# Kernel optimization log

Hardware: AMD Instinct MI355X
Metric: run time of the kernel (lower is better)

The kernel has to match this reference:

```python
import jax, jax.numpy as jnp
import numpy as np

N_NODES = 50000
N_EDGES = 800000
IN_CH = 128
HID_CH = 128   # factor(2) * out_channels(64)
OUT_CH = 64


def setup_inputs() -> dict:
    key = jax.random.key(0)
    k_x, k_e, k_w1, k_w2 = jax.random.split(key, 4)
    x = jax.random.normal(k_x, (N_NODES, IN_CH), dtype=jnp.float32)
    edge_index = jax.random.randint(k_e, (2, N_EDGES), 0, N_NODES, dtype=jnp.int32)
    # GCNConv weights (Glorot) and biases, layer1: in->2*out, layer2: 2*out->out
    s1 = float(np.sqrt(6.0 / (IN_CH + HID_CH)))
    s2 = float(np.sqrt(6.0 / (HID_CH + OUT_CH)))
    W1 = jax.random.uniform(k_w1, (IN_CH, HID_CH), jnp.float32, -s1, s1)
    b1 = jnp.zeros((HID_CH,), jnp.float32)
    W2 = jax.random.uniform(k_w2, (HID_CH, OUT_CH), jnp.float32, -s2, s2)
    b2 = jnp.zeros((OUT_CH,), jnp.float32)
    return {"x": x, "edge_index": edge_index, "W1": W1, "b1": b1, "W2": W2, "b2": b2}


def reference(x, edge_index, W1, b1, W2, b2):
    N = x.shape[0]
    src, dst = edge_index[0], edge_index[1]
    # add self loops (PyG GCNConv default)
    loop = jnp.arange(N, dtype=edge_index.dtype)
    src2 = jnp.concatenate([src, loop])
    dst2 = jnp.concatenate([dst, loop])
    # symmetric normalization D^-1/2 (A+I) D^-1/2
    deg = jax.ops.segment_sum(jnp.ones_like(src2, dtype=x.dtype), dst2, num_segments=N)
    deg_inv_sqrt = jnp.where(deg > 0, jax.lax.rsqrt(jnp.maximum(deg, 1e-12)), 0.0)
    norm = deg_inv_sqrt[src2] * deg_inv_sqrt[dst2]  # [E+N]

    def gcn_conv(h, W, b):
        h = h @ W                                   # [N, C_out]
        msg = h[src2] * norm[:, None]               # gather + scale
        agg = jax.ops.segment_sum(msg, dst2, num_segments=N)  # scatter-add
        return agg + b

    h = jax.nn.relu(gcn_conv(x, W1, b1))
    h = jax.nn.relu(gcn_conv(h, W2, b2))
    return h
```

## Files before the change

kernel.cpp:

```cpp
#include <hip/hip_runtime.h>
#include <math.h>

#define NN 50000
#define NE 800000
#define NB 391
#define CAP 4096
#define CHUNK 4096

typedef __attribute__((ext_vector_type(8))) short s8v;
typedef __attribute__((ext_vector_type(8))) unsigned short u16x8;
typedef __attribute__((ext_vector_type(4))) float f4v;

__device__ inline short bf16_rtn(float f) {
  unsigned u = __builtin_bit_cast(unsigned, f);
  u = (u + 0x7FFFu + ((u >> 16) & 1u)) >> 16;
  return (short)u;
}
__device__ inline float bf16_to_f(unsigned short h) {
  unsigned u = ((unsigned)h) << 16;
  return __builtin_bit_cast(float, u);
}

__global__ __launch_bounds__(512) void k_bucketA(const int* __restrict__ src,
                                                 const int* __restrict__ dst,
                                                 int* __restrict__ bcnt,
                                                 unsigned* __restrict__ ebuf, int E) {
  __shared__ int h[NB], lofs[NB], gbase[NB], lcur[NB];
  __shared__ unsigned staged[CHUNK];
  const int tid = threadIdx.x;
  const int e0 = blockIdx.x * CHUNK;
  const int nE = min(CHUNK, E - e0);
  for (int i = tid; i < NB; i += 512) { h[i] = 0; lcur[i] = 0; }
  __syncthreads();
  for (int i = tid; i < nE; i += 512) atomicAdd(&h[dst[e0 + i] >> 7], 1);
  __syncthreads();
  if (tid < 64) {
    int carry = 0;
    for (int c = 0; c < 7; ++c) {
      int idx = c * 64 + tid;
      int v = (idx < NB) ? h[idx] : 0;
      int s = v;
#pragma unroll
      for (int o = 1; o < 64; o <<= 1) {
        int t = __shfl_up(s, o);
        if (tid >= o) s += t;
      }
      if (idx < NB) lofs[idx] = carry + s - v;
      carry += __shfl(s, 63);
    }
  }
  __syncthreads();
  for (int i = tid; i < NB; i += 512)
    gbase[i] = h[i] ? (i * CAP + atomicAdd(&bcnt[i], h[i])) : 0;
  __syncthreads();
  for (int i = tid; i < nE; i += 512) {
    int d = dst[e0 + i];
    int s = src[e0 + i];
    int b = d >> 7;
    int pos = lofs[b] + atomicAdd(&lcur[b], 1);
    staged[pos] = ((unsigned)b << 23) | ((unsigned)(d & 127) << 16) | (unsigned)s;
  }
  __syncthreads();
  for (int i = tid; i < nE; i += 512) {
    unsigned v = staged[i];
    int b = v >> 23;
    ebuf[gbase[b] + (i - lofs[b])] = v;
  }
}

__global__ __launch_bounds__(256) void k_bucketB(const unsigned* __restrict__ ebuf,
                                                 const int* __restrict__ bcnt,
                                                 unsigned short* __restrict__ col,
                                                 int* __restrict__ rps,
                                                 int* __restrict__ rpe,
                                                 float* __restrict__ dinv) {
  __shared__ int h[128], ofs[128], lc[128];
  const int tid = threadIdx.x;
  const int b = blockIdx.x;
  const int base = b * CAP;
  const int cntE = bcnt[b];
  const int node0 = b << 7;
  const int nloc = min(128, NN - node0);
  if (tid < 128) { h[tid] = 0; lc[tid] = 0; }
  __syncthreads();
  for (int i = tid; i < cntE; i += 256) atomicAdd(&h[(ebuf[base + i] >> 16) & 127], 1);
  __syncthreads();
  if (tid < 64) {
    int carry = 0;
    for (int c = 0; c < 2; ++c) {
      int idx = c * 64 + tid;
      int v = h[idx];
      int s = v;
#pragma unroll
      for (int o = 1; o < 64; o <<= 1) {
        int t = __shfl_up(s, o);
        if (tid >= o) s += t;
      }
      ofs[idx] = carry + s - v;
      carry += __shfl(s, 63);
    }
  }
  __syncthreads();
  if (tid < nloc) {
    rps[node0 + tid] = base + ofs[tid];
    rpe[node0 + tid] = base + ofs[tid] + h[tid];
    dinv[node0 + tid] = rsqrtf((float)h[tid] + 1.0f);
  }
  __syncthreads();
  for (int i = tid; i < cntE; i += 256) {
    unsigned v = ebuf[base + i];
    int l = (v >> 16) & 127;
    int p = atomicAdd(&lc[l], 1);
    col[base + ofs[l] + p] = (unsigned short)(v & 0xFFFFu);
  }
}

template <int N>
__global__ __launch_bounds__(512) void k_gemm_mfma(const float* __restrict__ X,
                                                   const float* __restrict__ W,
                                                   const float* __restrict__ dinv,
                                                   unsigned short* __restrict__ H,
                                                   int M) {
  constexpr int NT = N / 16;
  constexpr int NSLOT = 4 * NT * 64;
  __shared__ short s_hi[NSLOT * 8];
  __shared__ short s_lo[NSLOT * 8];
  const int tid = threadIdx.x;

  for (int slot = tid; slot < NSLOT; slot += 512) {
    int lane = slot & 63;
    int frag = slot >> 6;
    int nt = frag % NT;
    int kt = frag / NT;
    int colb = nt * 16 + (lane & 15);
    int kb = kt * 32 + (lane >> 4) * 8;
    s8v hi, lo;
#pragma unroll
    for (int j = 0; j < 8; ++j) {
      float w = W[(size_t)(kb + j) * N + colb];
      short h = bf16_rtn(w);
      hi[j] = h;
      lo[j] = bf16_rtn(w - bf16_to_f((unsigned short)h));
    }
    *(s8v*)&s_hi[slot * 8] = hi;
    *(s8v*)&s_lo[slot * 8] = lo;
  }
  __syncthreads();

  const int wave = tid >> 6, lane = tid & 63;
  const int row0 = blockIdx.x * 128 + wave * 16;
  int arow = row0 + (lane & 15);
  if (arow >= M) arow = M - 1;
  const float* xr = X + (size_t)arow * 128 + (lane >> 4) * 8;

  f4v acc[NT];
#pragma unroll
  for (int nt = 0; nt < NT; ++nt) acc[nt] = (f4v){0.f, 0.f, 0.f, 0.f};

#pragma unroll
  for (int kt = 0; kt < 4; ++kt) {
    float4 a0 = *(const float4*)(xr + kt * 32);
    float4 a1 = *(const float4*)(xr + kt * 32 + 4);
    float af[8] = {a0.x, a0.y, a0.z, a0.w, a1.x, a1.y, a1.z, a1.w};
    s8v ah, al;
#pragma unroll
    for (int j = 0; j < 8; ++j) {
      short h = bf16_rtn(af[j]);
      ah[j] = h;
      al[j] = bf16_rtn(af[j] - bf16_to_f((unsigned short)h));
    }
#pragma unroll
    for (int nt = 0; nt < NT; ++nt) {
      int base = ((kt * NT + nt) * 64 + lane) * 8;
      s8v bh = *(const s8v*)&s_hi[base];
      s8v bl = *(const s8v*)&s_lo[base];
      acc[nt] = __builtin_amdgcn_mfma_f32_16x16x32_bf16(ah, bh, acc[nt], 0, 0, 0);
      acc[nt] = __builtin_amdgcn_mfma_f32_16x16x32_bf16(ah, bl, acc[nt], 0, 0, 0);
      acc[nt] = __builtin_amdgcn_mfma_f32_16x16x32_bf16(al, bh, acc[nt], 0, 0, 0);
    }
  }

  const int orow = row0 + (lane >> 4) * 4;
  const int ocol = lane & 15;
  float sc[4];
#pragma unroll
  for (int r = 0; r < 4; ++r) sc[r] = (orow + r < M) ? dinv[orow + r] : 0.f;
#pragma unroll
  for (int nt = 0; nt < NT; ++nt)
#pragma unroll
    for (int r = 0; r < 4; ++r)
      if (orow + r < M)
        H[(size_t)(orow + r) * N + nt * 16 + ocol] =
            (unsigned short)bf16_rtn(acc[nt][r] * sc[r]);
}

template <int N>
__global__ __launch_bounds__(512) void k_gemm_mfma_bf16A(
    const unsigned short* __restrict__ A, const float* __restrict__ W,
    const float* __restrict__ dinv, unsigned short* __restrict__ H, int M) {
  constexpr int NT = N / 16;
  constexpr int NSLOT = 4 * NT * 64;
  __shared__ short s_hi[NSLOT * 8];
  __shared__ short s_lo[NSLOT * 8];
  const int tid = threadIdx.x;

  for (int slot = tid; slot < NSLOT; slot += 512) {
    int lane = slot & 63;
    int frag = slot >> 6;
    int nt = frag % NT;
    int kt = frag / NT;
    int colb = nt * 16 + (lane & 15);
    int kb = kt * 32 + (lane >> 4) * 8;
    s8v hi, lo;
#pragma unroll
    for (int j = 0; j < 8; ++j) {
      float w = W[(size_t)(kb + j) * N + colb];
      short h = bf16_rtn(w);
      hi[j] = h;
      lo[j] = bf16_rtn(w - bf16_to_f((unsigned short)h));
    }
    *(s8v*)&s_hi[slot * 8] = hi;
    *(s8v*)&s_lo[slot * 8] = lo;
  }
  __syncthreads();

  const int wave = tid >> 6, lane = tid & 63;
  const int row0 = blockIdx.x * 128 + wave * 16;
  int arow = row0 + (lane & 15);
  if (arow >= M) arow = M - 1;
  const unsigned short* xr = A + (size_t)arow * 128 + (lane >> 4) * 8;

  f4v acc[NT];
#pragma unroll
  for (int nt = 0; nt < NT; ++nt) acc[nt] = (f4v){0.f, 0.f, 0.f, 0.f};

#pragma unroll
  for (int kt = 0; kt < 4; ++kt) {
    s8v ah = __builtin_bit_cast(s8v, *(const u16x8*)(xr + kt * 32));
#pragma unroll
    for (int nt = 0; nt < NT; ++nt) {
      int base = ((kt * NT + nt) * 64 + lane) * 8;
      s8v bh = *(const s8v*)&s_hi[base];
      s8v bl = *(const s8v*)&s_lo[base];
      acc[nt] = __builtin_amdgcn_mfma_f32_16x16x32_bf16(ah, bh, acc[nt], 0, 0, 0);
      acc[nt] = __builtin_amdgcn_mfma_f32_16x16x32_bf16(ah, bl, acc[nt], 0, 0, 0);
    }
  }

  const int orow = row0 + (lane >> 4) * 4;
  const int ocol = lane & 15;
  float sc[4];
#pragma unroll
  for (int r = 0; r < 4; ++r) sc[r] = (orow + r < M) ? dinv[orow + r] : 0.f;
#pragma unroll
  for (int nt = 0; nt < NT; ++nt)
#pragma unroll
    for (int r = 0; r < 4; ++r)
      if (orow + r < M)
        H[(size_t)(orow + r) * N + nt * 16 + ocol] =
            (unsigned short)bf16_rtn(acc[nt][r] * sc[r]);
}

template <int COUT, bool STORE_BF16>
__global__ __launch_bounds__(256) void k_agg(const unsigned short* __restrict__ H,
                                             const unsigned short* __restrict__ col,
                                             const int* __restrict__ rps,
                                             const int* __restrict__ rpe,
                                             const float* __restrict__ dinv,
                                             const float* __restrict__ bias,
                                             void* __restrict__ outv, int n) {
  const int TPN = COUT / 8;
  const int NPB = 256 / TPN;
  int node = blockIdx.x * NPB + threadIdx.x / TPN;
  int cg = (threadIdx.x % TPN) * 8;
  if (node >= n) return;
  float di = dinv[node];
  float acc[8];
  u16x8 hv = *(const u16x8*)(H + (size_t)node * COUT + cg);
#pragma unroll
  for (int q = 0; q < 8; ++q) acc[q] = bf16_to_f(hv[q]);
  int j = rps[node];
  int end = rpe[node];
  for (; j + 4 <= end; j += 4) {
    int s0 = col[j + 0], s1 = col[j + 1], s2 = col[j + 2], s3 = col[j + 3];
    u16x8 a = *(const u16x8*)(H + (size_t)s0 * COUT + cg);
    u16x8 b = *(const u16x8*)(H + (size_t)s1 * COUT + cg);
    u16x8 c = *(const u16x8*)(H + (size_t)s2 * COUT + cg);
    u16x8 d = *(const u16x8*)(H + (size_t)s3 * COUT + cg);
#pragma unroll
    for (int q = 0; q < 8; ++q)
      acc[q] += bf16_to_f(a[q]) + bf16_to_f(b[q]) + bf16_to_f(c[q]) + bf16_to_f(d[q]);
  }
  for (; j < end; ++j) {
    u16x8 a = *(const u16x8*)(H + (size_t)col[j] * COUT + cg);
#pragma unroll
    for (int q = 0; q < 8; ++q) acc[q] += bf16_to_f(a[q]);
  }
  float4 bv0 = *(const float4*)(bias + cg);
  float4 bv1 = *(const float4*)(bias + cg + 4);
  float r[8];
  r[0] = acc[0] * di + bv0.x; r[1] = acc[1] * di + bv0.y;
  r[2] = acc[2] * di + bv0.z; r[3] = acc[3] * di + bv0.w;
  r[4] = acc[4] * di + bv1.x; r[5] = acc[5] * di + bv1.y;
  r[6] = acc[6] * di + bv1.z; r[7] = acc[7] * di + bv1.w;
#pragma unroll
  for (int q = 0; q < 8; ++q) r[q] = r[q] > 0.f ? r[q] : 0.f;
  if (STORE_BF16) {
    u16x8 o;
#pragma unroll
    for (int q = 0; q < 8; ++q) o[q] = (unsigned short)bf16_rtn(r[q]);
    *(u16x8*)((unsigned short*)outv + (size_t)node * COUT + cg) = o;
  } else {
    float* out = (float*)outv;
    *(float4*)(out + (size_t)node * COUT + cg) = make_float4(r[0], r[1], r[2], r[3]);
    *(float4*)(out + (size_t)node * COUT + cg + 4) = make_float4(r[4], r[5], r[6], r[7]);
  }
}

extern "C" void kernel_launch(void* const* d_in, const int* in_sizes, int n_in,
                              void* d_out, int out_size, void* d_ws, size_t ws_size,
                              hipStream_t stream) {
  const float* x  = (const float*)d_in[0];
  const int*   ei = (const int*)d_in[1];
  const float* W1 = (const float*)d_in[2];
  const float* b1 = (const float*)d_in[3];
  const float* W2 = (const float*)d_in[4];
  const float* b2 = (const float*)d_in[5];
  float* out = (float*)d_out;

  const int N = NN, E = NE;
  const int* src = ei;
  const int* dst = ei + E;

  char* ws = (char*)d_ws;
  size_t off = 0;
  auto carve = [&](size_t bytes) -> void* {
    void* p = ws + off;
    off = (off + bytes + 255) & ~(size_t)255;
    return p;
  };
  int*            bcnt = (int*)carve((size_t)NB * 4);
  unsigned short* col  = (unsigned short*)carve((size_t)NB * CAP * 2);
  int*            rps  = (int*)carve((size_t)N * 4);
  int*            rpe  = (int*)carve((size_t)N * 4);
  float*          dinv = (float*)carve((size_t)N * 4);
  unsigned short* A1   = (unsigned short*)carve((size_t)N * 128 * 2);
  char*           R1   = (char*)carve((size_t)N * 128 * 2);
  unsigned*       ebuf = (unsigned*)R1;
  unsigned short* H1   = (unsigned short*)R1;
  unsigned short* H2   = (unsigned short*)R1;

  hipMemsetAsync(bcnt, 0, (size_t)NB * 4, stream);

  k_bucketA<<<(E + CHUNK - 1) / CHUNK, 512, 0, stream>>>(src, dst, bcnt, ebuf, E);
  k_bucketB<<<NB, 256, 0, stream>>>(ebuf, bcnt, col, rps, rpe, dinv);

  const int GB = (NN + 127) / 128;

  k_gemm_mfma<128><<<GB, 512, 0, stream>>>(x, W1, dinv, H1, N);
  k_agg<128, true><<<(N + 15) / 16, 256, 0, stream>>>(H1, col, rps, rpe, dinv, b1, A1, N);

  k_gemm_mfma_bf16A<64><<<GB, 512, 0, stream>>>(A1, W2, dinv, H2, N);
  k_agg<64, false><<<(N + 31) / 32, 256, 0, stream>>>(H2, col, rps, rpe, dinv, b2, out, N);
}
```

Measured before the change: 106.1 us.

## Fuse layer-1 aggregation with layer-2 GEMM via shared-memory tile

Merges the first aggregation kernel and the second-layer GEMM into one kernel. Each 16-node block aggregates into a bf16 tile in LDS, then runs MFMA against W2, which every block converts to bf16 in LDS. This removes the A1 round trip through global memory and one kernel launch. It also drops the hi/lo split of W2, so W2 is now single bf16, which costs precision. The price is redundant W2 conversion in each of the 3125 blocks, and the shared-memory footprint may reduce occupancy.

New measurement: 95.20 us. 1.11x faster.

```diff
diff --git a/kernel.cpp b/kernel.cpp
--- a/kernel.cpp
+++ b/kernel.cpp
@@ -194,105 +194,117 @@
             (unsigned short)bf16_rtn(acc[nt][r] * sc[r]);
 }
 
-template <int N>
-__global__ __launch_bounds__(512) void k_gemm_mfma_bf16A(
-    const unsigned short* __restrict__ A, const float* __restrict__ W,
-    const float* __restrict__ dinv, unsigned short* __restrict__ H, int M) {
-  constexpr int NT = N / 16;
-  constexpr int NSLOT = 4 * NT * 64;
-  __shared__ short s_hi[NSLOT * 8];
-  __shared__ short s_lo[NSLOT * 8];
+__global__ __launch_bounds__(256) void k_agg1_gemm2(
+    const unsigned short* __restrict__ H1, const unsigned short* __restrict__ col,
+    const int* __restrict__ rps, const int* __restrict__ rpe,
+    const float* __restrict__ dinv, const float* __restrict__ b1,
+    const float* __restrict__ W2, unsigned short* __restrict__ H2) {
+  __shared__ unsigned short s_w2[1024 * 8];
+  __shared__ unsigned short s_a1[16 * 136];
   const int tid = threadIdx.x;
 
-  for (int slot = tid; slot < NSLOT; slot += 512) {
+  for (int slot = tid; slot < 1024; slot += 256) {
     int lane = slot & 63;
     int frag = slot >> 6;
-    int nt = frag % NT;
-    int kt = frag / NT;
+    int nt = frag & 3;
+    int kt = frag >> 2;
     int colb = nt * 16 + (lane & 15);
     int kb = kt * 32 + (lane >> 4) * 8;
-    s8v hi, lo;
-#pragma unroll
-    for (int j = 0; j < 8; ++j) {
-      float w = W[(size_t)(kb + j) * N + colb];
-      short h = bf16_rtn(w);
-      hi[j] = h;
-      lo[j] = bf16_rtn(w - bf16_to_f((unsigned short)h));
-    }
-    *(s8v*)&s_hi[slot * 8] = hi;
-    *(s8v*)&s_lo[slot * 8] = lo;
-  }
-  __syncthreads();
-
-  const int wave = tid >> 6, lane = tid & 63;
-  const int row0 = blockIdx.x * 128 + wave * 16;
-  int arow = row0 + (lane & 15);
-  if (arow >= M) arow = M - 1;
-  const unsigned short* xr = A + (size_t)arow * 128 + (lane >> 4) * 8;
-
-  f4v acc[NT];
-#pragma unroll
-  for (int nt = 0; nt < NT; ++nt) acc[nt] = (f4v){0.f, 0.f, 0.f, 0.f};
-
-#pragma unroll
-  for (int kt = 0; kt < 4; ++kt) {
-    s8v ah = __builtin_bit_cast(s8v, *(const u16x8*)(xr + kt * 32));
-#pragma unroll
-    for (int nt = 0; nt < NT; ++nt) {
-      int base = ((kt * NT + nt) * 64 + lane) * 8;
-      s8v bh = *(const s8v*)&s_hi[base];
-      s8v bl = *(const s8v*)&s_lo[base];
-      acc[nt] = __builtin_amdgcn_mfma_f32_16x16x32_bf16(ah, bh, acc[nt], 0, 0, 0);
-      acc[nt] = __builtin_amdgcn_mfma_f32_16x16x32_bf16(ah, bl, acc[nt], 0, 0, 0);
-    }
-  }
-
-  const int orow = row0 + (lane >> 4) * 4;
-  const int ocol = lane & 15;
-  float sc[4];
-#pragma unroll
-  for (int r = 0; r < 4; ++r) sc[r] = (orow + r < M) ? dinv[orow + r] : 0.f;
-#pragma unroll
-  for (int nt = 0; nt < NT; ++nt)
-#pragma unroll
-    for (int r = 0; r < 4; ++r)
-      if (orow + r < M)
-        H[(size_t)(orow + r) * N + nt * 16 + ocol] =
-            (unsigned short)bf16_rtn(acc[nt][r] * sc[r]);
-}
-
-template <int COUT, bool STORE_BF16>
-__global__ __launch_bounds__(256) void k_agg(const unsigned short* __restrict__ H,
-                                             const unsigned short* __restrict__ col,
-                                             const int* __restrict__ rps,
-                                             const int* __restrict__ rpe,
-                                             const float* __restrict__ dinv,
-                                             const float* __restrict__ bias,
-                                             void* __restrict__ outv, int n) {
-  const int TPN = COUT / 8;
-  const int NPB = 256 / TPN;
-  int node = blockIdx.x * NPB + threadIdx.x / TPN;
-  int cg = (threadIdx.x % TPN) * 8;
-  if (node >= n) return;
+    u16x8 hi;
+#pragma unroll
+    for (int j = 0; j < 8; ++j)
+      hi[j] = (unsigned short)bf16_rtn(W2[(size_t)(kb + j) * 64 + colb]);
+    *(u16x8*)&s_w2[slot * 8] = hi;
+  }
+
+  const int ln = tid >> 4;
+  const int node = blockIdx.x * 16 + ln;
+  const int cg = (tid & 15) * 8;
   float di = dinv[node];
   float acc[8];
-  u16x8 hv = *(const u16x8*)(H + (size_t)node * COUT + cg);
+  u16x8 hv = *(const u16x8*)(H1 + (size_t)node * 128 + cg);
 #pragma unroll
   for (int q = 0; q < 8; ++q) acc[q] = bf16_to_f(hv[q]);
   int j = rps[node];
   int end = rpe[node];
   for (; j + 4 <= end; j += 4) {
     int s0 = col[j + 0], s1 = col[j + 1], s2 = col[j + 2], s3 = col[j + 3];
-    u16x8 a = *(const u16x8*)(H + (size_t)s0 * COUT + cg);
-    u16x8 b = *(const u16x8*)(H + (size_t)s1 * COUT + cg);
-    u16x8 c = *(const u16x8*)(H + (size_t)s2 * COUT + cg);
-    u16x8 d = *(const u16x8*)(H + (size_t)s3 * COUT + cg);
+    u16x8 a = *(const u16x8*)(H1 + (size_t)s0 * 128 + cg);
+    u16x8 b = *(const u16x8*)(H1 + (size_t)s1 * 128 + cg);
+    u16x8 c = *(const u16x8*)(H1 + (size_t)s2 * 128 + cg);
+    u16x8 d = *(const u16x8*)(H1 + (size_t)s3 * 128 + cg);
 #pragma unroll
     for (int q = 0; q < 8; ++q)
       acc[q] += bf16_to_f(a[q]) + bf16_to_f(b[q]) + bf16_to_f(c[q]) + bf16_to_f(d[q]);
   }
   for (; j < end; ++j) {
-    u16x8 a = *(const u16x8*)(H + (size_t)col[j] * COUT + cg);
+    u16x8 a = *(const u16x8*)(H1 + (size_t)col[j] * 128 + cg);
+#pragma unroll
+    for (int q = 0; q < 8; ++q) acc[q] += bf16_to_f(a[q]);
+  }
+  float4 bv0 = *(const float4*)(b1 + cg);
+  float4 bv1 = *(const float4*)(b1 + cg + 4);
+  float r[8];
+  r[0] = acc[0] * di + bv0.x; r[1] = acc[1] * di + bv0.y;
+  r[2] = acc[2] * di + bv0.z; r[3] = acc[3] * di + bv0.w;
+  r[4] = acc[4] * di + bv1.x; r[5] = acc[5] * di + bv1.y;
+  r[6] = acc[6] * di + bv1.z; r[7] = acc[7] * di + bv1.w;
+  u16x8 o;
+#pragma unroll
+  for (int q = 0; q < 8; ++q)
+    o[q] = (unsigned short)bf16_rtn(r[q] > 0.f ? r[q] : 0.f);
+  *(u16x8*)&s_a1[ln * 136 + cg] = o;
+  __syncthreads();
+
+  const int wave = tid >> 6, lane = tid & 63;
+  f4v cacc = (f4v){0.f, 0.f, 0.f, 0.f};
+#pragma unroll
+  for (int kt = 0; kt < 4; ++kt) {
+    s8v ah = __builtin_bit_cast(
+        s8v, *(const u16x8*)&s_a1[(lane & 15) * 136 + kt * 32 + (lane >> 4) * 8]);
+    s8v bh = *(const s8v*)&s_w2[((kt * 4 + wave) * 64 + lane) * 8];
+    cacc = __builtin_amdgcn_mfma_f32_16x16x32_bf16(ah, bh, cacc, 0, 0, 0);
+  }
+  const int node0 = blockIdx.x * 16;
+  const int orow = (lane >> 4) * 4;
+  const int ocol = lane & 15;
+#pragma unroll
+  for (int rr = 0; rr < 4; ++rr) {
+    int nd = node0 + orow + rr;
+    H2[(size_t)nd * 64 + wave * 16 + ocol] =
+        (unsigned short)bf16_rtn(cacc[rr] * dinv[nd]);
+  }
+}
+
+__global__ __launch_bounds__(256) void k_agg2(const unsigned short* __restrict__ H,
+                                              const unsigned short* __restrict__ col,
+                                              const int* __restrict__ rps,
+                                              const int* __restrict__ rpe,
+                                              const float* __restrict__ dinv,
+                                              const float* __restrict__ bias,
+                                              float* __restrict__ out, int n) {
+  int node = blockIdx.x * 32 + threadIdx.x / 8;
+  int cg = (threadIdx.x % 8) * 8;
+  if (node >= n) return;
+  float di = dinv[node];
+  float acc[8];
+  u16x8 hv = *(const u16x8*)(H + (size_t)node * 64 + cg);
+#pragma unroll
+  for (int q = 0; q < 8; ++q) acc[q] = bf16_to_f(hv[q]);
+  int j = rps[node];
+  int end = rpe[node];
+  for (; j + 4 <= end; j += 4) {
+    int s0 = col[j + 0], s1 = col[j + 1], s2 = col[j + 2], s3 = col[j + 3];
+    u16x8 a = *(const u16x8*)(H + (size_t)s0 * 64 + cg);
+    u16x8 b = *(const u16x8*)(H + (size_t)s1 * 64 + cg);
+    u16x8 c = *(const u16x8*)(H + (size_t)s2 * 64 + cg);
+    u16x8 d = *(const u16x8*)(H + (size_t)s3 * 64 + cg);
+#pragma unroll
+    for (int q = 0; q < 8; ++q)
+      acc[q] += bf16_to_f(a[q]) + bf16_to_f(b[q]) + bf16_to_f(c[q]) + bf16_to_f(d[q]);
+  }
+  for (; j < end; ++j) {
+    u16x8 a = *(const u16x8*)(H + (size_t)col[j] * 64 + cg);
 #pragma unroll
     for (int q = 0; q < 8; ++q) acc[q] += bf16_to_f(a[q]);
   }
@@ -305,16 +317,8 @@
   r[6] = acc[6] * di + bv1.z; r[7] = acc[7] * di + bv1.w;
 #pragma unroll
   for (int q = 0; q < 8; ++q) r[q] = r[q] > 0.f ? r[q] : 0.f;
-  if (STORE_BF16) {
-    u16x8 o;
-#pragma unroll
-    for (int q = 0; q < 8; ++q) o[q] = (unsigned short)bf16_rtn(r[q]);
-    *(u16x8*)((unsigned short*)outv + (size_t)node * COUT + cg) = o;
-  } else {
-    float* out = (float*)outv;
-    *(float4*)(out + (size_t)node * COUT + cg) = make_float4(r[0], r[1], r[2], r[3]);
-    *(float4*)(out + (size_t)node * COUT + cg + 4) = make_float4(r[4], r[5], r[6], r[7]);
-  }
+  *(float4*)(out + (size_t)node * 64 + cg) = make_float4(r[0], r[1], r[2], r[3]);
+  *(float4*)(out + (size_t)node * 64 + cg + 4) = make_float4(r[4], r[5], r[6], r[7]);
 }
 
 extern "C" void kernel_launch(void* const* d_in, const int* in_sizes, int n_in,
@@ -344,11 +348,10 @@
   int*            rps  = (int*)carve((size_t)N * 4);
   int*            rpe  = (int*)carve((size_t)N * 4);
   float*          dinv = (float*)carve((size_t)N * 4);
-  unsigned short* A1   = (unsigned short*)carve((size_t)N * 128 * 2);
+  unsigned short* H2   = (unsigned short*)carve((size_t)N * 64 * 2);
   char*           R1   = (char*)carve((size_t)N * 128 * 2);
   unsigned*       ebuf = (unsigned*)R1;
   unsigned short* H1   = (unsigned short*)R1;
-  unsigned short* H2   = (unsigned short*)R1;
 
   hipMemsetAsync(bcnt, 0, (size_t)NB * 4, stream);
 
@@ -358,8 +361,8 @@
   const int GB = (NN + 127) / 128;
 
   k_gemm_mfma<128><<<GB, 512, 0, stream>>>(x, W1, dinv, H1, N);
-  k_agg<128, true><<<(N + 15) / 16, 256, 0, stream>>>(H1, col, rps, rpe, dinv, b1, A1, N);
-
-  k_gemm_mfma_bf16A<64><<<GB, 512, 0, stream>>>(A1, W2, dinv, H2, N);
-  k_agg<64, false><<<(N + 31) / 32, 256, 0, stream>>>(H2, col, rps, rpe, dinv, b2, out, N);
-}
+
+  k_agg1_gemm2<<<NN / 16, 256, 0, stream>>>(H1, col, rps, rpe, dinv, b1, W2, H2);
+
+  k_agg2<<<(N + 31) / 32, 256, 0, stream>>>(H2, col, rps, rpe, dinv, b2, out, N);
+}
```
